# Kernel optimization log

Measured on AMD Instinct MI355X. Metric: run time of the kernel, lower is better.

The kernel has to match this reference:

```python
import jax, jax.numpy as jnp
import numpy as np

N_NODES = 50000
N_FEAT = 128
N_HIDDEN = 256
N_CLASSES = 1
N_EDGES = 800000


def gcn_layer(x, src, dst, W, b, n_nodes):
    """GCNConv: D^-1/2 (A + I) D^-1/2 X W + b, via gather-scatter over edges."""
    h = x @ W  # [N, out]
    # add self loops
    loop = jnp.arange(n_nodes, dtype=src.dtype)
    s = jnp.concatenate([src, loop])
    d = jnp.concatenate([dst, loop])
    deg = jax.ops.segment_sum(jnp.ones_like(d, dtype=h.dtype), d, num_segments=n_nodes)
    inv_sqrt = jax.lax.rsqrt(jnp.maximum(deg, 1.0))
    norm = inv_sqrt[s] * inv_sqrt[d]  # [E+N]
    msgs = h[s] * norm[:, None]       # gather: [E+N, out]
    out = jax.ops.segment_sum(msgs, d, num_segments=n_nodes)  # scatter-add
    return out + b


def setup_inputs() -> dict:
    key = jax.random.key(0)
    k1, k2, k3, k4 = jax.random.split(key, 4)
    x = jax.random.normal(k1, (N_NODES, N_FEAT), dtype=jnp.float32)
    edge_index = jax.random.randint(k2, (2, N_EDGES), 0, N_NODES, dtype=jnp.int32)
    s1 = 1.0 / np.sqrt(N_FEAT)
    s2 = 1.0 / np.sqrt(N_HIDDEN)
    W1 = jax.random.uniform(k3, (N_FEAT, N_HIDDEN), jnp.float32, -s1, s1)
    b1 = jnp.zeros((N_HIDDEN,), jnp.float32)
    W2 = jax.random.uniform(k4, (N_HIDDEN, N_CLASSES), jnp.float32, -s2, s2)
    b2 = jnp.zeros((N_CLASSES,), jnp.float32)
    return {"x": x, "edge_index": edge_index, "W1": W1, "b1": b1, "W2": W2, "b2": b2}


def reference(x, edge_index, W1, b1, W2, b2):
    src, dst = edge_index[0], edge_index[1]
    n = x.shape[0]
    h = gcn_layer(x, src, dst, W1, b1, n)
    h = jax.nn.relu(h)  # dropout=0.0 -> identity
    out = gcn_layer(h, src, dst, W2, b2, n)
    return out  # [N, n_classes]
```

## Files before the change

### kernel.cpp

```cpp
#include <hip/hip_runtime.h>

typedef unsigned int uint;
typedef unsigned short ushort;
typedef __attribute__((ext_vector_type(8))) short short8;
typedef __attribute__((ext_vector_type(4))) float f32x4;

#define CAP   64
#define BM16  16
#define STR   68
#define NPB   192
#define NBIN  261
#define CAPB  4096
#define EPB   4096

__device__ __forceinline__ float bf_lo(uint p) { return __uint_as_float(p << 16); }
__device__ __forceinline__ float bf_hi(uint p) { return __uint_as_float(p & 0xffff0000u); }
__device__ __forceinline__ uint rne_lo(uint u) { return (u + 0x7fffu + ((u >> 16) & 1u)) >> 16; }
__device__ __forceinline__ uint rne_hi(uint u) { return (u + 0x7fffu + ((u >> 16) & 1u)) & 0xffff0000u; }

__global__ __launch_bounds__(1024) void k_part(
    const int* __restrict__ src, const int* __restrict__ dst,
    int* __restrict__ binCnt, uint* __restrict__ binData, int E) {
  __shared__ int hist[NBIN];
  __shared__ int base[NBIN];
  int t = threadIdx.x;
  for (int i = t; i < NBIN; i += 1024) hist[i] = 0;
  __syncthreads();
  int s[4], d[4], b[4];
  bool v[4];
#pragma unroll
  for (int j = 0; j < 4; ++j) {
    int e = blockIdx.x * EPB + j * 1024 + t;
    v[j] = e < E;
    if (v[j]) {
      s[j] = src[e];
      d[j] = dst[e];
      b[j] = d[j] / NPB;
      atomicAdd(&hist[b[j]], 1);
    }
  }
  __syncthreads();
  for (int i = t; i < NBIN; i += 1024) {
    int h = hist[i];
    base[i] = h ? atomicAdd(&binCnt[i], h) : 0;
    hist[i] = 0;
  }
  __syncthreads();
#pragma unroll
  for (int j = 0; j < 4; ++j) {
    if (v[j]) {
      int r = atomicAdd(&hist[b[j]], 1);
      int idx = base[b[j]] + r;
      if (idx < CAPB)
        binData[b[j] * CAPB + idx] = (uint)s[j] | ((uint)d[j] << 16);
    }
  }
}

__global__ __launch_bounds__(1024) void k_bucketize(
    const uint* __restrict__ binData, const int* __restrict__ binCnt,
    ushort* __restrict__ col, int* __restrict__ cnt, int N) {
  __shared__ ushort col_l[NPB * CAP];
  __shared__ int cnt_l[NPB];
  int b = blockIdx.x, t = threadIdx.x;
  int lo = b * NPB;
  for (int i = t; i < NPB; i += 1024) cnt_l[i] = 0;
  __syncthreads();
  int m = min(binCnt[b], CAPB);
  const uint* bd = &binData[b * CAPB];
  for (int e = t; e < m; e += 1024) {
    uint pr = bd[e];
    int sv = pr & 0xffffu;
    int dl = (int)(pr >> 16) - lo;
    int p = atomicAdd(&cnt_l[dl], 1);
    if (p < CAP) col_l[dl * CAP + p] = (ushort)sv;
  }
  __syncthreads();
  int nh = min(NPB, N - lo);
  if (nh <= 0) return;
  for (int i = t; i < nh; i += 1024) cnt[lo + i] = cnt_l[i];
  uint* cg = (uint*)(col + (size_t)lo * CAP);
  const uint* cl = (const uint*)col_l;
  int nu = nh * (CAP / 2);
  for (int i = t; i < nu; i += 1024) cg[i] = cl[i];
}

__global__ void k_prep2(const float2* __restrict__ x2, const int* __restrict__ cnt,
                        uint* __restrict__ xs, float* __restrict__ inv,
                        const float* __restrict__ W1, uint* __restrict__ wpack,
                        int N, int nconv) {
  int gid = blockIdx.x * blockDim.x + threadIdx.x;
  if (gid < 4096) {
    int kk = gid >> 10, rem = gid & 1023, ntile = rem >> 6, ln = rem & 63;
    int quad = ln >> 4, nn = ntile * 16 + (ln & 15);
    uint d[4];
#pragma unroll
    for (int jp = 0; jp < 4; ++jp) {
      int k = kk * 32 + quad * 8 + 2 * jp;
      uint lov = rne_lo(__float_as_uint(W1[k * 256 + nn]));
      uint hiv = rne_hi(__float_as_uint(W1[(k + 1) * 256 + nn]));
      d[jp] = lov | hiv;
    }
    *(uint4*)&wpack[gid * 4] = make_uint4(d[0], d[1], d[2], d[3]);
  } else if (gid < 4096 + N) {
    int i = gid - 4096;
    inv[i] = rsqrtf((float)(cnt[i] + 1));
  } else if (gid < 4096 + N + nconv) {
    int cid = gid - 4096 - N;
    int node = cid >> 6;
    float invd = rsqrtf((float)(cnt[node] + 1));
    float2 f = x2[cid];
    xs[cid] = rne_lo(__float_as_uint(invd * f.x)) | rne_hi(__float_as_uint(invd * f.y));
  }
}

__global__ __launch_bounds__(256, 2) void k_agg_gemm(
    const uint* __restrict__ xs, const ushort* __restrict__ col,
    const int* __restrict__ cnt, const float* __restrict__ inv,
    const uint* __restrict__ wpack, const float* __restrict__ b1,
    const float* __restrict__ W2, float* __restrict__ cz, int N) {
  __shared__ uint As[BM16 * STR];
  __shared__ float red[64];
  int t = threadIdx.x, wave = t >> 6, lane = t & 63;
  int m0 = blockIdx.x * BM16;

  for (int rr = 0; rr < 4; ++rr) {
    int m = wave * 4 + rr;
    int node = m0 + m;
    float2 acc = make_float2(0.f, 0.f);
    if (node < N) {
      uint pd = xs[(size_t)node * 64 + lane];
      acc.x = bf_lo(pd);
      acc.y = bf_hi(pd);
      int e = min(cnt[node], CAP);
      int ce = (int)col[node * CAP + lane];
      int p = 0;
      for (; p + 15 < e; p += 16) {
        uint pv[16];
#pragma unroll
        for (int j = 0; j < 16; ++j) {
          int s = __shfl(ce, p + j);
          pv[j] = xs[(size_t)s * 64 + lane];
        }
#pragma unroll
        for (int j = 0; j < 16; ++j) { acc.x += bf_lo(pv[j]); acc.y += bf_hi(pv[j]); }
      }
      for (; p + 3 < e; p += 4) {
        uint pv[4];
#pragma unroll
        for (int j = 0; j < 4; ++j) {
          int s = __shfl(ce, p + j);
          pv[j] = xs[(size_t)s * 64 + lane];
        }
#pragma unroll
        for (int j = 0; j < 4; ++j) { acc.x += bf_lo(pv[j]); acc.y += bf_hi(pv[j]); }
      }
      for (; p < e; ++p) {
        int s = __shfl(ce, p);
        uint p0 = xs[(size_t)s * 64 + lane];
        acc.x += bf_lo(p0); acc.y += bf_hi(p0);
      }
      float invd = inv[node];
      acc.x *= invd;
      acc.y *= invd;
    }
    As[m * STR + lane] = rne_lo(__float_as_uint(acc.x)) | rne_hi(__float_as_uint(acc.y));
  }
  __syncthreads();

  int quad = lane >> 4, mrow = lane & 15;
  f32x4 acc[4];
#pragma unroll
  for (int nt = 0; nt < 4; ++nt) acc[nt] = (f32x4){0.f, 0.f, 0.f, 0.f};
#pragma unroll
  for (int kk = 0; kk < 4; ++kk) {
    short8 af = *(const short8*)&As[mrow * STR + kk * 16 + quad * 4];
#pragma unroll
    for (int nt = 0; nt < 4; ++nt) {
      int ntile = wave * 4 + nt;
      short8 bf = *(const short8*)&wpack[((kk * 16 + ntile) * 64 + lane) * 4];
      acc[nt] = __builtin_amdgcn_mfma_f32_16x16x32_bf16(af, bf, acc[nt], 0, 0, 0);
    }
  }

  float partial[4] = {0.f, 0.f, 0.f, 0.f};
#pragma unroll
  for (int nt = 0; nt < 4; ++nt) {
    int c = (wave * 4 + nt) * 16 + mrow;
    float b1c = b1[c], w2c = W2[c];
#pragma unroll
    for (int r = 0; r < 4; ++r) {
      float h = fmaxf(acc[nt][r] + b1c, 0.f);
      partial[r] = fmaf(h, w2c, partial[r]);
    }
  }
#pragma unroll
  for (int r = 0; r < 4; ++r) {
    float p = partial[r];
    p += __shfl_xor(p, 1); p += __shfl_xor(p, 2);
    p += __shfl_xor(p, 4); p += __shfl_xor(p, 8);
    if (mrow == 0) red[wave * 16 + quad * 4 + r] = p;
  }
  __syncthreads();
  if (t < 16) {
    int node = m0 + t;
    if (node < N) {
      float s = red[t] + red[16 + t] + red[32 + t] + red[48 + t];
      cz[node] = inv[node] * s;
    }
  }
}

__global__ void k_agg2(const ushort* __restrict__ col, const int* __restrict__ cnt,
                       const float* __restrict__ cz, const float* __restrict__ b2,
                       float* __restrict__ out, int N) {
  int g = blockIdx.x * blockDim.x + threadIdx.x;
  int node = g >> 2, q = g & 3;
  if (node >= N) return;
  int e = min(cnt[node], CAP);
  float acc = (q == 0) ? cz[node] : 0.f;
  const ushort* cp = &col[node * CAP];
  for (int p = q; p < e; p += 4) acc += cz[cp[p]];
  acc += __shfl_xor(acc, 1);
  acc += __shfl_xor(acc, 2);
  if (q == 0) out[node] = rsqrtf((float)(cnt[node] + 1)) * acc + b2[0];
}

extern "C" void kernel_launch(void* const* d_in, const int* in_sizes, int n_in,
                              void* d_out, int out_size, void* d_ws, size_t ws_size,
                              hipStream_t stream) {
  const float2* x2 = (const float2*)d_in[0];
  const int*    ei = (const int*)d_in[1];
  const float*  W1 = (const float*)d_in[2];
  const float*  b1 = (const float*)d_in[3];
  const float*  W2 = (const float*)d_in[4];
  const float*  b2 = (const float*)d_in[5];
  int N = in_sizes[0] / 128;
  int E = in_sizes[1] / 2;
  const int* src = ei;
  const int* dst = ei + E;
  float* out = (float*)d_out;

  char* w = (char*)d_ws;
  size_t o = 0;
  auto carve = [&](size_t bytes) { char* p = w + o; o += (bytes + 255) & ~(size_t)255; return p; };
  int*    binCnt  = (int*)   carve((size_t)NBIN * 4);
  int*    cnt     = (int*)   carve((size_t)N * 4);
  uint*   binData = (uint*)  carve((size_t)NBIN * CAPB * 4);
  ushort* col     = (ushort*)carve((size_t)N * CAP * 2);
  uint*   xs      = (uint*)  carve((size_t)N * 64 * 4);
  float*  inv     = (float*) carve((size_t)N * 4);
  uint*   wpack   = (uint*)  carve(16384 * 4);
  float*  cz      = (float*) carve((size_t)N * 4);

  hipMemsetAsync(binCnt, 0, (size_t)NBIN * sizeof(int), stream);

  int nblk_p = (E + EPB - 1) / EPB;
  k_part<<<nblk_p, 1024, 0, stream>>>(src, dst, binCnt, binData, E);

  k_bucketize<<<NBIN, 1024, 0, stream>>>(binData, binCnt, col, cnt, N);

  int nconv = N * 64;
  int tprep = 4096 + N + nconv;
  k_prep2<<<(tprep + 255) / 256, 256, 0, stream>>>(x2, cnt, xs, inv, W1, wpack, N, nconv);

  k_agg_gemm<<<(N + BM16 - 1) / BM16, 256, 0, stream>>>(
      xs, col, cnt, inv, wpack, b1, W2, cz, N);

  long long tot2 = (long long)N * 4;
  k_agg2<<<(int)((tot2 + 255) / 256), 256, 0, stream>>>(col, cnt, cz, b2, out, N);
}
```

Baseline: 144.5 us.

## Fold prep kernel into partition and bucketize kernels

Removes the separate k_prep2 launch. W1 packing into bf16 tiles now runs in 16 extra blocks appended to the partition kernel, and the per-node inverse sqrt degree plus the scaled bf16 feature conversion now run in the bucketize kernel, which reads the degree counts from shared memory. k_agg2 reuses the precomputed inv array. This cuts one launch and a global read of cnt, at the cost of heavier bucketize blocks: only 261 blocks now do the 50000x64 feature conversion, so the conversion has less parallelism.

```diff
diff --git a/kernel.cpp b/kernel.cpp
--- a/kernel.cpp
+++ b/kernel.cpp
@@ -20,10 +20,28 @@
 
 __global__ __launch_bounds__(1024) void k_part(
     const int* __restrict__ src, const int* __restrict__ dst,
-    int* __restrict__ binCnt, uint* __restrict__ binData, int E) {
+    int* __restrict__ binCnt, uint* __restrict__ binData,
+    const float* __restrict__ W1, uint* __restrict__ wpack, int E, int nblk_e) {
+  int t = threadIdx.x;
+  if ((int)blockIdx.x >= nblk_e) {
+    int g = ((int)blockIdx.x - nblk_e) * 256 + (t & 255);
+    if ((t >> 8) == 0 && g < 4096) {
+      int kk = g >> 10, rem = g & 1023, ntile = rem >> 6, ln = rem & 63;
+      int quad = ln >> 4, nn = ntile * 16 + (ln & 15);
+      uint d[4];
+#pragma unroll
+      for (int jp = 0; jp < 4; ++jp) {
+        int k = kk * 32 + quad * 8 + 2 * jp;
+        uint lov = rne_lo(__float_as_uint(W1[k * 256 + nn]));
+        uint hiv = rne_hi(__float_as_uint(W1[(k + 1) * 256 + nn]));
+        d[jp] = lov | hiv;
+      }
+      *(uint4*)&wpack[g * 4] = make_uint4(d[0], d[1], d[2], d[3]);
+    }
+    return;
+  }
   __shared__ int hist[NBIN];
   __shared__ int base[NBIN];
-  int t = threadIdx.x;
   for (int i = t; i < NBIN; i += 1024) hist[i] = 0;
   __syncthreads();
   int s[4], d[4], b[4];
@@ -59,7 +77,9 @@
 
 __global__ __launch_bounds__(1024) void k_bucketize(
     const uint* __restrict__ binData, const int* __restrict__ binCnt,
-    ushort* __restrict__ col, int* __restrict__ cnt, int N) {
+    ushort* __restrict__ col, int* __restrict__ cnt,
+    const float2* __restrict__ x2, uint* __restrict__ xs, float* __restrict__ inv,
+    int N) {
   __shared__ ushort col_l[NPB * CAP];
   __shared__ int cnt_l[NPB];
   int b = blockIdx.x, t = threadIdx.x;
@@ -78,39 +98,22 @@
   __syncthreads();
   int nh = min(NPB, N - lo);
   if (nh <= 0) return;
-  for (int i = t; i < nh; i += 1024) cnt[lo + i] = cnt_l[i];
+  for (int i = t; i < nh; i += 1024) {
+    int c = cnt_l[i];
+    cnt[lo + i] = c;
+    inv[lo + i] = rsqrtf((float)(c + 1));
+  }
   uint* cg = (uint*)(col + (size_t)lo * CAP);
   const uint* cl = (const uint*)col_l;
   int nu = nh * (CAP / 2);
   for (int i = t; i < nu; i += 1024) cg[i] = cl[i];
-}
-
-__global__ void k_prep2(const float2* __restrict__ x2, const int* __restrict__ cnt,
-                        uint* __restrict__ xs, float* __restrict__ inv,
-                        const float* __restrict__ W1, uint* __restrict__ wpack,
-                        int N, int nconv) {
-  int gid = blockIdx.x * blockDim.x + threadIdx.x;
-  if (gid < 4096) {
-    int kk = gid >> 10, rem = gid & 1023, ntile = rem >> 6, ln = rem & 63;
-    int quad = ln >> 4, nn = ntile * 16 + (ln & 15);
-    uint d[4];
-#pragma unroll
-    for (int jp = 0; jp < 4; ++jp) {
-      int k = kk * 32 + quad * 8 + 2 * jp;
-      uint lov = rne_lo(__float_as_uint(W1[k * 256 + nn]));
-      uint hiv = rne_hi(__float_as_uint(W1[(k + 1) * 256 + nn]));
-      d[jp] = lov | hiv;
-    }
-    *(uint4*)&wpack[gid * 4] = make_uint4(d[0], d[1], d[2], d[3]);
-  } else if (gid < 4096 + N) {
-    int i = gid - 4096;
-    inv[i] = rsqrtf((float)(cnt[i] + 1));
-  } else if (gid < 4096 + N + nconv) {
-    int cid = gid - 4096 - N;
-    int node = cid >> 6;
-    float invd = rsqrtf((float)(cnt[node] + 1));
-    float2 f = x2[cid];
-    xs[cid] = rne_lo(__float_as_uint(invd * f.x)) | rne_hi(__float_as_uint(invd * f.y));
+  int nc = nh * 64;
+  for (int i = t; i < nc; i += 1024) {
+    int node = lo + (i >> 6);
+    float invd = rsqrtf((float)(cnt_l[i >> 6] + 1));
+    float2 f = x2[(size_t)node * 64 + (i & 63)];
+    xs[(size_t)node * 64 + (i & 63)] =
+        rne_lo(__float_as_uint(invd * f.x)) | rne_hi(__float_as_uint(invd * f.y));
   }
 }
 
@@ -212,8 +215,8 @@
 }
 
 __global__ void k_agg2(const ushort* __restrict__ col, const int* __restrict__ cnt,
-                       const float* __restrict__ cz, const float* __restrict__ b2,
-                       float* __restrict__ out, int N) {
+                       const float* __restrict__ inv, const float* __restrict__ cz,
+                       const float* __restrict__ b2, float* __restrict__ out, int N) {
   int g = blockIdx.x * blockDim.x + threadIdx.x;
   int node = g >> 2, q = g & 3;
   if (node >= N) return;
@@ -223,7 +226,7 @@
   for (int p = q; p < e; p += 4) acc += cz[cp[p]];
   acc += __shfl_xor(acc, 1);
   acc += __shfl_xor(acc, 2);
-  if (q == 0) out[node] = rsqrtf((float)(cnt[node] + 1)) * acc + b2[0];
+  if (q == 0) out[node] = inv[node] * acc + b2[0];
 }
 
 extern "C" void kernel_launch(void* const* d_in, const int* in_sizes, int n_in,
@@ -255,18 +258,14 @@
 
   hipMemsetAsync(binCnt, 0, (size_t)NBIN * sizeof(int), stream);
 
-  int nblk_p = (E + EPB - 1) / EPB;
-  k_part<<<nblk_p, 1024, 0, stream>>>(src, dst, binCnt, binData, E);
-
-  k_bucketize<<<NBIN, 1024, 0, stream>>>(binData, binCnt, col, cnt, N);
-
-  int nconv = N * 64;
-  int tprep = 4096 + N + nconv;
-  k_prep2<<<(tprep + 255) / 256, 256, 0, stream>>>(x2, cnt, xs, inv, W1, wpack, N, nconv);
+  int nblk_e = (E + EPB - 1) / EPB;
+  k_part<<<nblk_e + 16, 1024, 0, stream>>>(src, dst, binCnt, binData, W1, wpack, E, nblk_e);
+
+  k_bucketize<<<NBIN, 1024, 0, stream>>>(binData, binCnt, col, cnt, x2, xs, inv, N);
 
   k_agg_gemm<<<(N + BM16 - 1) / BM16, 256, 0, stream>>>(
       xs, col, cnt, inv, wpack, b1, W2, cz, N);
 
   long long tot2 = (long long)N * 4;
-  k_agg2<<<(int)((tot2 + 255) / 256), 256, 0, stream>>>(col, cnt, cz, b2, out, N);
-}
+  k_agg2<<<(int)((tot2 + 255) / 256), 256, 0, stream>>>(col, cnt, inv, cz, b2, out, N);
+}
```

Result: no change. 147.3 us (+2.0%).

## Replace global-atomic bin partition with per-block local partitions and histograms

Applied to the files above, without the earlier changes.

Edge partitioning now writes each block's edges into its own contiguous slice, ordered by destination bin. A wave-level prefix scan over the local histogram gives the offsets, and the per-block histograms and offsets are stored for later use. Bucketize then walks every partition block's segment for its bin, one wave per partition block. This removes the global atomics on the bin counters, the memset and the fixed per-bin cap. In exchange, bucketize now does many small strided reads over 196 partition segments, which risks poorly coalesced short loops.

```diff
diff --git a/kernel.cpp b/kernel.cpp
--- a/kernel.cpp
+++ b/kernel.cpp
@@ -10,7 +10,6 @@
 #define STR   68
 #define NPB   192
 #define NBIN  261
-#define CAPB  4096
 #define EPB   4096
 
 __device__ __forceinline__ float bf_lo(uint p) { return __uint_as_float(p << 16); }
@@ -20,17 +19,19 @@
 
 __global__ __launch_bounds__(1024) void k_part(
     const int* __restrict__ src, const int* __restrict__ dst,
-    int* __restrict__ binCnt, uint* __restrict__ binData, int E) {
+    uint* __restrict__ partData, ushort* __restrict__ hist196,
+    ushort* __restrict__ off196, int E) {
   __shared__ int hist[NBIN];
-  __shared__ int base[NBIN];
-  int t = threadIdx.x;
-  for (int i = t; i < NBIN; i += 1024) hist[i] = 0;
+  __shared__ int off[NBIN];
+  __shared__ int cursor[NBIN];
+  int t = threadIdx.x, bx = (int)blockIdx.x;
+  for (int i = t; i < NBIN; i += 1024) { hist[i] = 0; cursor[i] = 0; }
   __syncthreads();
   int s[4], d[4], b[4];
   bool v[4];
 #pragma unroll
   for (int j = 0; j < 4; ++j) {
-    int e = blockIdx.x * EPB + j * 1024 + t;
+    int e = bx * EPB + j * 1024 + t;
     v[j] = e < E;
     if (v[j]) {
       s[j] = src[e];
@@ -40,40 +41,55 @@
     }
   }
   __syncthreads();
-  for (int i = t; i < NBIN; i += 1024) {
-    int h = hist[i];
-    base[i] = h ? atomicAdd(&binCnt[i], h) : 0;
-    hist[i] = 0;
+  if (t < 64) {
+    int running = 0;
+    for (int base = 0; base < NBIN; base += 64) {
+      int idx = base + t;
+      int h = (idx < NBIN) ? hist[idx] : 0;
+      int sc = h;
+#pragma unroll
+      for (int o2 = 1; o2 < 64; o2 <<= 1) {
+        int tmp = __shfl_up(sc, o2);
+        if (t >= o2) sc += tmp;
+      }
+      if (idx < NBIN) off[idx] = running + sc - h;
+      running += __shfl(sc, 63);
+    }
   }
   __syncthreads();
 #pragma unroll
   for (int j = 0; j < 4; ++j) {
     if (v[j]) {
-      int r = atomicAdd(&hist[b[j]], 1);
-      int idx = base[b[j]] + r;
-      if (idx < CAPB)
-        binData[b[j] * CAPB + idx] = (uint)s[j] | ((uint)d[j] << 16);
-    }
+      int r = atomicAdd(&cursor[b[j]], 1);
+      partData[bx * EPB + off[b[j]] + r] = (uint)s[j] | ((uint)d[j] << 16);
+    }
+  }
+  for (int i = t; i < NBIN; i += 1024) {
+    hist196[bx * NBIN + i] = (ushort)hist[i];
+    off196[bx * NBIN + i] = (ushort)off[i];
   }
 }
 
 __global__ __launch_bounds__(1024) void k_bucketize(
-    const uint* __restrict__ binData, const int* __restrict__ binCnt,
-    ushort* __restrict__ col, int* __restrict__ cnt, int N) {
+    const uint* __restrict__ partData, const ushort* __restrict__ hist196,
+    const ushort* __restrict__ off196, ushort* __restrict__ col,
+    int* __restrict__ cnt, int N, int nblk_e) {
   __shared__ ushort col_l[NPB * CAP];
   __shared__ int cnt_l[NPB];
-  int b = blockIdx.x, t = threadIdx.x;
+  int b = (int)blockIdx.x, t = threadIdx.x, wave = t >> 6, lane = t & 63;
   int lo = b * NPB;
   for (int i = t; i < NPB; i += 1024) cnt_l[i] = 0;
   __syncthreads();
-  int m = min(binCnt[b], CAPB);
-  const uint* bd = &binData[b * CAPB];
-  for (int e = t; e < m; e += 1024) {
-    uint pr = bd[e];
-    int sv = pr & 0xffffu;
-    int dl = (int)(pr >> 16) - lo;
-    int p = atomicAdd(&cnt_l[dl], 1);
-    if (p < CAP) col_l[dl * CAP + p] = (ushort)sv;
+  for (int pb = wave; pb < nblk_e; pb += 16) {
+    int h  = (int)hist196[pb * NBIN + b];
+    int of = (int)off196[pb * NBIN + b];
+    for (int l2 = lane; l2 < h; l2 += 64) {
+      uint pr = partData[pb * EPB + of + l2];
+      int sv = pr & 0xffffu;
+      int dl = (int)(pr >> 16) - lo;
+      int p = atomicAdd(&cnt_l[dl], 1);
+      if (p < CAP) col_l[dl * CAP + p] = (ushort)sv;
+    }
   }
   __syncthreads();
   int nh = min(NPB, N - lo);
@@ -241,24 +257,25 @@
   const int* dst = ei + E;
   float* out = (float*)d_out;
 
+  int nblk_e = (E + EPB - 1) / EPB;
+
   char* w = (char*)d_ws;
   size_t o = 0;
   auto carve = [&](size_t bytes) { char* p = w + o; o += (bytes + 255) & ~(size_t)255; return p; };
-  int*    binCnt  = (int*)   carve((size_t)NBIN * 4);
-  int*    cnt     = (int*)   carve((size_t)N * 4);
-  uint*   binData = (uint*)  carve((size_t)NBIN * CAPB * 4);
-  ushort* col     = (ushort*)carve((size_t)N * CAP * 2);
-  uint*   xs      = (uint*)  carve((size_t)N * 64 * 4);
-  float*  inv     = (float*) carve((size_t)N * 4);
-  uint*   wpack   = (uint*)  carve(16384 * 4);
-  float*  cz      = (float*) carve((size_t)N * 4);
-
-  hipMemsetAsync(binCnt, 0, (size_t)NBIN * sizeof(int), stream);
-
-  int nblk_p = (E + EPB - 1) / EPB;
-  k_part<<<nblk_p, 1024, 0, stream>>>(src, dst, binCnt, binData, E);
-
-  k_bucketize<<<NBIN, 1024, 0, stream>>>(binData, binCnt, col, cnt, N);
+  uint*   partData = (uint*)  carve((size_t)nblk_e * EPB * 4);
+  ushort* hist196  = (ushort*)carve((size_t)nblk_e * NBIN * 2);
+  ushort* off196   = (ushort*)carve((size_t)nblk_e * NBIN * 2);
+  int*    cnt      = (int*)   carve((size_t)N * 4);
+  ushort* col      = (ushort*)carve((size_t)N * CAP * 2);
+  uint*   xs       = (uint*)  carve((size_t)N * 64 * 4);
+  float*  inv      = (float*) carve((size_t)N * 4);
+  uint*   wpack    = (uint*)  carve(16384 * 4);
+  float*  cz       = (float*) carve((size_t)N * 4);
+
+
+  k_part<<<nblk_e, 1024, 0, stream>>>(src, dst, partData, hist196, off196, E);
+
+  k_bucketize<<<NBIN, 1024, 0, stream>>>(partData, hist196, off196, col, cnt, N, nblk_e);
 
   int nconv = N * 64;
   int tprep = 4096 + N + nconv;
```

New measurement: 147.7 us. 2.2% more time.
